# Performance work log

Measured on AMD Instinct MI355X. Metric: run time of the kernel, lower is better.

## Reference

```python
import jax, jax.numpy as jnp
import numpy as np

LN_EPS = 1e-6  # flax nn.LayerNorm default epsilon
NEG_SLOPE = 0.01  # jax.nn.leaky_relu default


def _layer_norm(x, scale, bias):
    m = jnp.mean(x, axis=-1, keepdims=True)
    v = jnp.mean(jnp.square(x - m), axis=-1, keepdims=True)
    return (x - m) * jax.lax.rsqrt(v + LN_EPS) * scale + bias


def setup_inputs() -> dict:
    key = jax.random.key(0)
    ks = jax.random.split(key, 10)
    B, D1, D2, OUT = 32768, 1024, 512, 1024
    inp = {
        "x1": jax.random.normal(ks[0], (B, D1), dtype=jnp.float32),
        "x2": jax.random.normal(ks[1], (B, D2), dtype=jnp.float32),
        # LayerNorm params (one per stream)
        "ln_scale1": jnp.ones((D1,), jnp.float32),
        "ln_bias1": jnp.zeros((D1,), jnp.float32),
        "ln_scale2": jnp.ones((D2,), jnp.float32),
        "ln_bias2": jnp.zeros((D2,), jnp.float32),
        # output Dense per stream: Dense(output_size)
        "W_out1": jax.random.normal(ks[2], (D1, OUT), jnp.float32) / np.sqrt(D1),
        "b_out1": jnp.zeros((OUT,), jnp.float32),
        "W_out2": jax.random.normal(ks[3], (D2, OUT), jnp.float32) / np.sqrt(D2),
        "b_out2": jnp.zeros((OUT,), jnp.float32),
        # gate Dense per stream: Dense(gate_size=output_size) for POINTWISE
        "W_g1": jax.random.normal(ks[4], (D1, OUT), jnp.float32) / np.sqrt(D1),
        "b_g1": jnp.zeros((OUT,), jnp.float32),
        "W_g2": jax.random.normal(ks[5], (D2, OUT), jnp.float32) / np.sqrt(D2),
        "b_g2": jnp.zeros((OUT,), jnp.float32),
    }
    return inp


def reference(x1, x2, ln_scale1, ln_bias1, ln_scale2, ln_bias2,
              W_out1, b_out1, W_out2, b_out2,
              W_g1, b_g1, W_g2, b_g2):
    # per-stream: LayerNorm -> leaky_relu -> Dense(output_size); pre-Dense
    # activation is also fed to the gate Dense.
    f1 = jax.nn.leaky_relu(_layer_norm(x1, ln_scale1, ln_bias1), NEG_SLOPE)
    f2 = jax.nn.leaky_relu(_layer_norm(x2, ln_scale2, ln_bias2), NEG_SLOPE)
    out1 = f1 @ W_out1 + b_out1  # [B, OUT]
    out2 = f2 @ W_out2 + b_out2  # [B, OUT]
    # two-stream POINTWISE gate: sum of gate Denses, sigmoid; the original
    # broadcasts gate [B,OUT] over stack([out1,out2]) and sums axis 0,
    # i.e. output = gate * (out1 + out2).
    gate = jax.nn.sigmoid((f1 @ W_g1 + b_g1) + (f2 @ W_g2 + b_g2))
    return gate * (out1 + out2)
```

## Files before the change

### kernel.cpp

```cpp
#include <hip/hip_runtime.h>
#include <hip/hip_bf16.h>
#include <stdint.h>

typedef __bf16 bf16x8 __attribute__((ext_vector_type(8)));
typedef float floatx4 __attribute__((ext_vector_type(4)));

__device__ __forceinline__ ushort f2bf(float f) {
  union { float f; uint32_t u; } v; v.f = f;
  uint32_t r = (v.u + 0x7fffu + ((v.u >> 16) & 1u)) >> 16;
  return (ushort)r;
}

__device__ __forceinline__ void load_lds16(const ushort* g, ushort* l) {
  __builtin_amdgcn_global_load_lds(
      (__attribute__((address_space(1))) void*)g,
      (__attribute__((address_space(3))) void*)l, 16, 0, 0);
}

__device__ __forceinline__ float leaky(float x) { return x >= 0.f ? x : 0.01f * x; }

__global__ __launch_bounds__(256) void ln2_kernel(
    const float* __restrict__ x1, const float* __restrict__ x2,
    const float* __restrict__ sc1p, const float* __restrict__ bi1p,
    const float* __restrict__ sc2p, const float* __restrict__ bi2p,
    ushort* __restrict__ f) {
  const int wid = (blockIdx.x << 2) + (threadIdx.x >> 6);
  const int lane = threadIdx.x & 63;

  float4 sc1[4], bi1[4], sc2[2], bi2[2];
#pragma unroll
  for (int j = 0; j < 4; j++) {
    sc1[j] = ((const float4*)sc1p)[j * 64 + lane];
    bi1[j] = ((const float4*)bi1p)[j * 64 + lane];
  }
#pragma unroll
  for (int j = 0; j < 2; j++) {
    sc2[j] = ((const float4*)sc2p)[j * 64 + lane];
    bi2[j] = ((const float4*)bi2p)[j * 64 + lane];
  }

#pragma unroll
  for (int it = 0; it < 2; ++it) {
    const int rA = wid + it * 16384;
    const int rB = rA + 8192;
    const float4* XA1 = (const float4*)(x1 + (size_t)rA * 1024);
    const float4* XA2 = (const float4*)(x2 + (size_t)rA * 512);
    const float4* XB1 = (const float4*)(x1 + (size_t)rB * 1024);
    const float4* XB2 = (const float4*)(x2 + (size_t)rB * 512);
    float4 a1[4], a2[2], b1[4], b2[2];
#pragma unroll
    for (int j = 0; j < 4; j++) a1[j] = XA1[j * 64 + lane];
#pragma unroll
    for (int j = 0; j < 2; j++) a2[j] = XA2[j * 64 + lane];
#pragma unroll
    for (int j = 0; j < 4; j++) b1[j] = XB1[j * 64 + lane];
#pragma unroll
    for (int j = 0; j < 2; j++) b2[j] = XB2[j * 64 + lane];

    float sA1 = 0.f, qA1 = 0.f, sA2 = 0.f, qA2 = 0.f;
    float sB1 = 0.f, qB1 = 0.f, sB2 = 0.f, qB2 = 0.f;
#pragma unroll
    for (int j = 0; j < 4; j++) {
      sA1 += a1[j].x + a1[j].y + a1[j].z + a1[j].w;
      qA1 += a1[j].x * a1[j].x + a1[j].y * a1[j].y + a1[j].z * a1[j].z + a1[j].w * a1[j].w;
      sB1 += b1[j].x + b1[j].y + b1[j].z + b1[j].w;
      qB1 += b1[j].x * b1[j].x + b1[j].y * b1[j].y + b1[j].z * b1[j].z + b1[j].w * b1[j].w;
    }
#pragma unroll
    for (int j = 0; j < 2; j++) {
      sA2 += a2[j].x + a2[j].y + a2[j].z + a2[j].w;
      qA2 += a2[j].x * a2[j].x + a2[j].y * a2[j].y + a2[j].z * a2[j].z + a2[j].w * a2[j].w;
      sB2 += b2[j].x + b2[j].y + b2[j].z + b2[j].w;
      qB2 += b2[j].x * b2[j].x + b2[j].y * b2[j].y + b2[j].z * b2[j].z + b2[j].w * b2[j].w;
    }
#pragma unroll
    for (int o = 1; o < 64; o <<= 1) {
      sA1 += __shfl_xor(sA1, o); qA1 += __shfl_xor(qA1, o);
      sA2 += __shfl_xor(sA2, o); qA2 += __shfl_xor(qA2, o);
      sB1 += __shfl_xor(sB1, o); qB1 += __shfl_xor(qB1, o);
      sB2 += __shfl_xor(sB2, o); qB2 += __shfl_xor(qB2, o);
    }
    const float mA1 = sA1 * (1.0f / 1024.0f);
    const float rA1 = rsqrtf(qA1 * (1.0f / 1024.0f) - mA1 * mA1 + 1e-6f);
    const float mA2 = sA2 * (1.0f / 512.0f);
    const float rA2v = rsqrtf(qA2 * (1.0f / 512.0f) - mA2 * mA2 + 1e-6f);
    const float mB1 = sB1 * (1.0f / 1024.0f);
    const float rB1 = rsqrtf(qB1 * (1.0f / 1024.0f) - mB1 * mB1 + 1e-6f);
    const float mB2 = sB2 * (1.0f / 512.0f);
    const float rB2v = rsqrtf(qB2 * (1.0f / 512.0f) - mB2 * mB2 + 1e-6f);

    ushort* fA = f + (size_t)rA * 1536;
    ushort* fB = f + (size_t)rB * 1536;
#pragma unroll
    for (int j = 0; j < 4; j++) {
      ushort4 oA, oB;
      oA.x = f2bf(leaky((a1[j].x - mA1) * rA1 * sc1[j].x + bi1[j].x));
      oA.y = f2bf(leaky((a1[j].y - mA1) * rA1 * sc1[j].y + bi1[j].y));
      oA.z = f2bf(leaky((a1[j].z - mA1) * rA1 * sc1[j].z + bi1[j].z));
      oA.w = f2bf(leaky((a1[j].w - mA1) * rA1 * sc1[j].w + bi1[j].w));
      oB.x = f2bf(leaky((b1[j].x - mB1) * rB1 * sc1[j].x + bi1[j].x));
      oB.y = f2bf(leaky((b1[j].y - mB1) * rB1 * sc1[j].y + bi1[j].y));
      oB.z = f2bf(leaky((b1[j].z - mB1) * rB1 * sc1[j].z + bi1[j].z));
      oB.w = f2bf(leaky((b1[j].w - mB1) * rB1 * sc1[j].w + bi1[j].w));
      ((ushort4*)fA)[j * 64 + lane] = oA;
      ((ushort4*)fB)[j * 64 + lane] = oB;
    }
#pragma unroll
    for (int j = 0; j < 2; j++) {
      ushort4 oA, oB;
      oA.x = f2bf(leaky((a2[j].x - mA2) * rA2v * sc2[j].x + bi2[j].x));
      oA.y = f2bf(leaky((a2[j].y - mA2) * rA2v * sc2[j].y + bi2[j].y));
      oA.z = f2bf(leaky((a2[j].z - mA2) * rA2v * sc2[j].z + bi2[j].z));
      oA.w = f2bf(leaky((a2[j].w - mA2) * rA2v * sc2[j].w + bi2[j].w));
      oB.x = f2bf(leaky((b2[j].x - mB2) * rB2v * sc2[j].x + bi2[j].x));
      oB.y = f2bf(leaky((b2[j].y - mB2) * rB2v * sc2[j].y + bi2[j].y));
      oB.z = f2bf(leaky((b2[j].z - mB2) * rB2v * sc2[j].z + bi2[j].z));
      oB.w = f2bf(leaky((b2[j].w - mB2) * rB2v * sc2[j].w + bi2[j].w));
      ((ushort4*)(fA + 1024))[j * 64 + lane] = oA;
      ((ushort4*)(fB + 1024))[j * 64 + lane] = oB;
    }
  }
}

__global__ __launch_bounds__(256) void wprep_kernel(
    const float* __restrict__ Wo1, const float* __restrict__ Wo2,
    const float* __restrict__ Wg1, const float* __restrict__ Wg2,
    ushort* __restrict__ WT) {
  __shared__ float tile[32][33];
  const int k0 = blockIdx.x * 32;
  const int j0 = blockIdx.y * 32;
  const int s = blockIdx.z;
  const float* Wa = s ? Wg1 : Wo1;
  const float* Wb = s ? Wg2 : Wo2;
  const int tx = threadIdx.x;
  const int ty = threadIdx.y;
#pragma unroll
  for (int r = 0; r < 4; r++) {
    const int k = k0 + ty + 8 * r;
    const float val = (k < 1024) ? Wa[(size_t)k * 1024 + j0 + tx]
                                 : Wb[(size_t)(k - 1024) * 1024 + j0 + tx];
    tile[ty + 8 * r][tx] = val;
  }
  __syncthreads();
#pragma unroll
  for (int r = 0; r < 4; r++) {
    const int j = j0 + ty + 8 * r;
    const int c = j & 63;
    const int n = (j >> 6) * 128 + (c >> 5) * 64 + s * 32 + ((c >> 4) & 1) * 16 + (c & 15);
    WT[(size_t)n * 1536 + k0 + tx] = f2bf(tile[tx][ty + 8 * r]);
  }
}

__global__ __launch_bounds__(512, 2) void gemm_fused(
    const ushort* __restrict__ A,
    const ushort* __restrict__ Bt,
    const float* __restrict__ bo1, const float* __restrict__ bo2,
    const float* __restrict__ bg1, const float* __restrict__ bg2,
    float* __restrict__ out) {
  __shared__ __align__(16) ushort As[2][16384];
  __shared__ __align__(16) ushort Bs[2][16384];
  const int orig = blockIdx.x;
  const int swz = (orig & 7) * 128 + (orig >> 3);
  const int mt = swz >> 3;
  const int nt = swz & 7;
  const int tid = threadIdx.x;
  const int wave = tid >> 6, lane = tid & 63;
  const int wr = wave >> 2, wcol = wave & 3;
  const int low = lane & 15, quad = lane >> 4;

  const int srow = wave * 8 + (lane >> 3);
  const int schunk = (lane & 7) ^ (lane >> 3);
  const ushort* gA0 = A + ((size_t)mt * 256 + srow) * 1536 + schunk * 8;
  const ushort* gB0 = Bt + ((size_t)nt * 256 + srow) * 1536 + schunk * 8;

  const int q2 = quad ^ (low & 3);
  const int kx = (low >> 2) & 1;
  const int offA_k0 = (wr * 128 + low) * 64 + (q2 + 4 * kx) * 8;
  const int offA_k1 = (wr * 128 + low) * 64 + (q2 + 4 * (1 - kx)) * 8;
  const int offB_k0 = (wcol * 64 + low) * 64 + (q2 + 4 * kx) * 8;
  const int offB_k1 = (wcol * 64 + low) * 64 + (q2 + 4 * (1 - kx)) * 8;

  floatx4 acc[8][4];
#pragma unroll
  for (int m = 0; m < 8; m++)
#pragma unroll
    for (int n = 0; n < 4; n++) acc[m][n] = (floatx4)0.0f;

#define STAGE_A(BUF, KT) do { \
    const ushort* s_ = gA0 + (KT) * 64; \
    ushort* d_ = &As[BUF][wave * 512]; \
    load_lds16(s_, d_); \
    load_lds16(s_ + 64 * 1536, d_ + 4096); \
    load_lds16(s_ + 128 * 1536, d_ + 8192); \
    load_lds16(s_ + 192 * 1536, d_ + 12288); \
  } while (0)
#define STAGE_B(BUF, KT) do { \
    const ushort* s_ = gB0 + (KT) * 64; \
    ushort* d_ = &Bs[BUF][wave * 512]; \
    load_lds16(s_, d_); \
    load_lds16(s_ + 64 * 1536, d_ + 4096); \
    load_lds16(s_ + 128 * 1536, d_ + 8192); \
    load_lds16(s_ + 192 * 1536, d_ + 12288); \
  } while (0)

  STAGE_A(0, 0);
  STAGE_B(0, 0);
  asm volatile("s_waitcnt vmcnt(0)" ::: "memory");
  __builtin_amdgcn_s_barrier();
  asm volatile("" ::: "memory");

#define TILE_STEP(CUR, T) do { \
    const ushort* Ac = &As[CUR][0]; \
    const ushort* Bc = &Bs[CUR][0]; \
    const bool pf = (T) < 23; \
    bf16x8 a[4], b[4]; \
     \
    _Pragma("unroll") for (int m = 0; m < 4; m++) a[m] = *(const bf16x8*)(Ac + offA_k0 + m * 1024); \
    _Pragma("unroll") for (int n = 0; n < 4; n++) b[n] = *(const bf16x8*)(Bc + offB_k0 + n * 1024); \
    if (pf) STAGE_A((CUR) ^ 1, (T) + 1); \
    asm volatile("" ::: "memory"); \
    __builtin_amdgcn_s_barrier(); \
    __builtin_amdgcn_s_setprio(1); \
    _Pragma("unroll") for (int m = 0; m < 4; m++) \
      _Pragma("unroll") for (int n = 0; n < 4; n++) \
        acc[m][n] = __builtin_amdgcn_mfma_f32_16x16x32_bf16(a[m], b[n], acc[m][n], 0, 0, 0); \
    __builtin_amdgcn_s_setprio(0); \
    asm volatile("" ::: "memory"); \
    __builtin_amdgcn_s_barrier(); \
     \
    _Pragma("unroll") for (int m = 0; m < 4; m++) a[m] = *(const bf16x8*)(Ac + offA_k0 + (m + 4) * 1024); \
    if (pf) STAGE_B((CUR) ^ 1, (T) + 1); \
    asm volatile("" ::: "memory"); \
    __builtin_amdgcn_s_barrier(); \
    __builtin_amdgcn_s_setprio(1); \
    _Pragma("unroll") for (int m = 0; m < 4; m++) \
      _Pragma("unroll") for (int n = 0; n < 4; n++) \
        acc[m + 4][n] = __builtin_amdgcn_mfma_f32_16x16x32_bf16(a[m], b[n], acc[m + 4][n], 0, 0, 0); \
    __builtin_amdgcn_s_setprio(0); \
    asm volatile("" ::: "memory"); \
    __builtin_amdgcn_s_barrier(); \
     \
    _Pragma("unroll") for (int m = 0; m < 4; m++) a[m] = *(const bf16x8*)(Ac + offA_k1 + m * 1024); \
    _Pragma("unroll") for (int n = 0; n < 4; n++) b[n] = *(const bf16x8*)(Bc + offB_k1 + n * 1024); \
    asm volatile("" ::: "memory"); \
    __builtin_amdgcn_s_barrier(); \
    __builtin_amdgcn_s_setprio(1); \
    _Pragma("unroll") for (int m = 0; m < 4; m++) \
      _Pragma("unroll") for (int n = 0; n < 4; n++) \
        acc[m][n] = __builtin_amdgcn_mfma_f32_16x16x32_bf16(a[m], b[n], acc[m][n], 0, 0, 0); \
    __builtin_amdgcn_s_setprio(0); \
    asm volatile("" ::: "memory"); \
    __builtin_amdgcn_s_barrier(); \
     \
    _Pragma("unroll") for (int m = 0; m < 4; m++) a[m] = *(const bf16x8*)(Ac + offA_k1 + (m + 4) * 1024); \
    asm volatile("" ::: "memory"); \
    __builtin_amdgcn_s_barrier(); \
    __builtin_amdgcn_s_setprio(1); \
    _Pragma("unroll") for (int m = 0; m < 4; m++) \
      _Pragma("unroll") for (int n = 0; n < 4; n++) \
        acc[m + 4][n] = __builtin_amdgcn_mfma_f32_16x16x32_bf16(a[m], b[n], acc[m + 4][n], 0, 0, 0); \
    __builtin_amdgcn_s_setprio(0); \
    asm volatile("s_waitcnt vmcnt(0)" ::: "memory"); \
    __builtin_amdgcn_s_barrier(); \
    asm volatile("" ::: "memory"); \
  } while (0)

  for (int tt = 0; tt < 12; tt++) {
    TILE_STEP(0, 2 * tt);
    TILE_STEP(1, 2 * tt + 1);
  }
#undef TILE_STEP
#undef STAGE_A
#undef STAGE_B

  const int colbase = (nt * 4 + wcol) << 5;
#pragma unroll
  for (int n = 0; n < 2; n++) {
    const int col = colbase + n * 16 + low;
    const float bs = bo1[col] + bo2[col];
    const float bg = bg1[col] + bg2[col];
#pragma unroll
    for (int m = 0; m < 8; m++) {
      const floatx4 S = acc[m][n];
      const floatx4 G = acc[m][n + 2];
      const size_t rb = (size_t)mt * 256 + wr * 128 + m * 16 + quad * 4;
#pragma unroll
      for (int r = 0; r < 4; r++) {
        const float sv = S[r] + bs;
        const float gv = G[r] + bg;
        const float gate = 1.0f / (1.0f + __expf(-gv));
        out[(rb + r) * 1024 + col] = gate * sv;
      }
    }
  }
}

extern "C" void kernel_launch(void* const* d_in, const int* in_sizes, int n_in,
                              void* d_out, int out_size, void* d_ws, size_t ws_size,
                              hipStream_t stream) {
  const float* x1 = (const float*)d_in[0];
  const float* x2 = (const float*)d_in[1];
  const float* ln_s1 = (const float*)d_in[2];
  const float* ln_b1 = (const float*)d_in[3];
  const float* ln_s2 = (const float*)d_in[4];
  const float* ln_b2 = (const float*)d_in[5];
  const float* W_out1 = (const float*)d_in[6];
  const float* b_out1 = (const float*)d_in[7];
  const float* W_out2 = (const float*)d_in[8];
  const float* b_out2 = (const float*)d_in[9];
  const float* W_g1 = (const float*)d_in[10];
  const float* b_g1 = (const float*)d_in[11];
  const float* W_g2 = (const float*)d_in[12];
  const float* b_g2 = (const float*)d_in[13];
  float* out = (float*)d_out;

  ushort* f = (ushort*)d_ws;
  ushort* WT = f + (size_t)32768 * 1536;

  ln2_kernel<<<2048, 256, 0, stream>>>(x1, x2, ln_s1, ln_b1, ln_s2, ln_b2, f);
  wprep_kernel<<<dim3(48, 32, 2), dim3(32, 8), 0, stream>>>(W_out1, W_out2, W_g1, W_g2, WT);
  gemm_fused<<<dim3(1024), dim3(512), 0, stream>>>(f, WT, b_out1, b_out2, b_g1, b_g2, out);
}
```

Baseline: 518.4 us.

## Fuse LayerNorm apply into GEMM A-staging, keep only per-row stats pass

Replaces the LayerNorm kernel that wrote a bf16 activation matrix with a stats-only kernel that stores per-row mean and rstd. The GEMM now loads raw fp32 x1/x2 rows, applies normalization, leaky ReLU and bf16 packing in registers, and writes the result into LDS instead of using async global-to-LDS loads. This removes the write and re-read of the bf16 intermediate. In exchange, the GEMM reads fp32 A once per N tile (8 times, twice the bytes of bf16) and adds VALU work and register pressure to the main loop.

```diff
diff --git a/kernel.cpp b/kernel.cpp
--- a/kernel.cpp
+++ b/kernel.cpp
@@ -4,6 +4,7 @@
 
 typedef __bf16 bf16x8 __attribute__((ext_vector_type(8)));
 typedef float floatx4 __attribute__((ext_vector_type(4)));
+typedef unsigned short u16x8v __attribute__((ext_vector_type(8)));
 
 __device__ __forceinline__ ushort f2bf(float f) {
   union { float f; uint32_t u; } v; v.f = f;
@@ -19,26 +20,25 @@
 
 __device__ __forceinline__ float leaky(float x) { return x >= 0.f ? x : 0.01f * x; }
 
-__global__ __launch_bounds__(256) void ln2_kernel(
+__device__ __forceinline__ u16x8v lnpack(float4 xa, float4 xb, float4 sa, float4 sb,
+                                         float4 ba, float4 bb, float m, float rv) {
+  u16x8v o;
+  o[0] = f2bf(leaky((xa.x - m) * rv * sa.x + ba.x));
+  o[1] = f2bf(leaky((xa.y - m) * rv * sa.y + ba.y));
+  o[2] = f2bf(leaky((xa.z - m) * rv * sa.z + ba.z));
+  o[3] = f2bf(leaky((xa.w - m) * rv * sa.w + ba.w));
+  o[4] = f2bf(leaky((xb.x - m) * rv * sb.x + bb.x));
+  o[5] = f2bf(leaky((xb.y - m) * rv * sb.y + bb.y));
+  o[6] = f2bf(leaky((xb.z - m) * rv * sb.z + bb.z));
+  o[7] = f2bf(leaky((xb.w - m) * rv * sb.w + bb.w));
+  return o;
+}
+
+__global__ __launch_bounds__(256) void stats_kernel(
     const float* __restrict__ x1, const float* __restrict__ x2,
-    const float* __restrict__ sc1p, const float* __restrict__ bi1p,
-    const float* __restrict__ sc2p, const float* __restrict__ bi2p,
-    ushort* __restrict__ f) {
+    float* __restrict__ stats) {
   const int wid = (blockIdx.x << 2) + (threadIdx.x >> 6);
   const int lane = threadIdx.x & 63;
-
-  float4 sc1[4], bi1[4], sc2[2], bi2[2];
-#pragma unroll
-  for (int j = 0; j < 4; j++) {
-    sc1[j] = ((const float4*)sc1p)[j * 64 + lane];
-    bi1[j] = ((const float4*)bi1p)[j * 64 + lane];
-  }
-#pragma unroll
-  for (int j = 0; j < 2; j++) {
-    sc2[j] = ((const float4*)sc2p)[j * 64 + lane];
-    bi2[j] = ((const float4*)bi2p)[j * 64 + lane];
-  }
-
 #pragma unroll
   for (int it = 0; it < 2; ++it) {
     const int rA = wid + it * 16384;
@@ -47,31 +47,25 @@
     const float4* XA2 = (const float4*)(x2 + (size_t)rA * 512);
     const float4* XB1 = (const float4*)(x1 + (size_t)rB * 1024);
     const float4* XB2 = (const float4*)(x2 + (size_t)rB * 512);
-    float4 a1[4], a2[2], b1[4], b2[2];
-#pragma unroll
-    for (int j = 0; j < 4; j++) a1[j] = XA1[j * 64 + lane];
-#pragma unroll
-    for (int j = 0; j < 2; j++) a2[j] = XA2[j * 64 + lane];
-#pragma unroll
-    for (int j = 0; j < 4; j++) b1[j] = XB1[j * 64 + lane];
-#pragma unroll
-    for (int j = 0; j < 2; j++) b2[j] = XB2[j * 64 + lane];
-
     float sA1 = 0.f, qA1 = 0.f, sA2 = 0.f, qA2 = 0.f;
     float sB1 = 0.f, qB1 = 0.f, sB2 = 0.f, qB2 = 0.f;
 #pragma unroll
     for (int j = 0; j < 4; j++) {
-      sA1 += a1[j].x + a1[j].y + a1[j].z + a1[j].w;
-      qA1 += a1[j].x * a1[j].x + a1[j].y * a1[j].y + a1[j].z * a1[j].z + a1[j].w * a1[j].w;
-      sB1 += b1[j].x + b1[j].y + b1[j].z + b1[j].w;
-      qB1 += b1[j].x * b1[j].x + b1[j].y * b1[j].y + b1[j].z * b1[j].z + b1[j].w * b1[j].w;
+      const float4 a = XA1[j * 64 + lane];
+      const float4 b = XB1[j * 64 + lane];
+      sA1 += a.x + a.y + a.z + a.w;
+      qA1 += a.x * a.x + a.y * a.y + a.z * a.z + a.w * a.w;
+      sB1 += b.x + b.y + b.z + b.w;
+      qB1 += b.x * b.x + b.y * b.y + b.z * b.z + b.w * b.w;
     }
 #pragma unroll
     for (int j = 0; j < 2; j++) {
-      sA2 += a2[j].x + a2[j].y + a2[j].z + a2[j].w;
-      qA2 += a2[j].x * a2[j].x + a2[j].y * a2[j].y + a2[j].z * a2[j].z + a2[j].w * a2[j].w;
-      sB2 += b2[j].x + b2[j].y + b2[j].z + b2[j].w;
-      qB2 += b2[j].x * b2[j].x + b2[j].y * b2[j].y + b2[j].z * b2[j].z + b2[j].w * b2[j].w;
+      const float4 a = XA2[j * 64 + lane];
+      const float4 b = XB2[j * 64 + lane];
+      sA2 += a.x + a.y + a.z + a.w;
+      qA2 += a.x * a.x + a.y * a.y + a.z * a.z + a.w * a.w;
+      sB2 += b.x + b.y + b.z + b.w;
+      qB2 += b.x * b.x + b.y * b.y + b.z * b.z + b.w * b.w;
     }
 #pragma unroll
     for (int o = 1; o < 64; o <<= 1) {
@@ -80,44 +74,17 @@
       sB1 += __shfl_xor(sB1, o); qB1 += __shfl_xor(qB1, o);
       sB2 += __shfl_xor(sB2, o); qB2 += __shfl_xor(qB2, o);
     }
-    const float mA1 = sA1 * (1.0f / 1024.0f);
-    const float rA1 = rsqrtf(qA1 * (1.0f / 1024.0f) - mA1 * mA1 + 1e-6f);
-    const float mA2 = sA2 * (1.0f / 512.0f);
-    const float rA2v = rsqrtf(qA2 * (1.0f / 512.0f) - mA2 * mA2 + 1e-6f);
-    const float mB1 = sB1 * (1.0f / 1024.0f);
-    const float rB1 = rsqrtf(qB1 * (1.0f / 1024.0f) - mB1 * mB1 + 1e-6f);
-    const float mB2 = sB2 * (1.0f / 512.0f);
-    const float rB2v = rsqrtf(qB2 * (1.0f / 512.0f) - mB2 * mB2 + 1e-6f);
-
-    ushort* fA = f + (size_t)rA * 1536;
-    ushort* fB = f + (size_t)rB * 1536;
-#pragma unroll
-    for (int j = 0; j < 4; j++) {
-      ushort4 oA, oB;
-      oA.x = f2bf(leaky((a1[j].x - mA1) * rA1 * sc1[j].x + bi1[j].x));
-      oA.y = f2bf(leaky((a1[j].y - mA1) * rA1 * sc1[j].y + bi1[j].y));
-      oA.z = f2bf(leaky((a1[j].z - mA1) * rA1 * sc1[j].z + bi1[j].z));
-      oA.w = f2bf(leaky((a1[j].w - mA1) * rA1 * sc1[j].w + bi1[j].w));
-      oB.x = f2bf(leaky((b1[j].x - mB1) * rB1 * sc1[j].x + bi1[j].x));
-      oB.y = f2bf(leaky((b1[j].y - mB1) * rB1 * sc1[j].y + bi1[j].y));
-      oB.z = f2bf(leaky((b1[j].z - mB1) * rB1 * sc1[j].z + bi1[j].z));
-      oB.w = f2bf(leaky((b1[j].w - mB1) * rB1 * sc1[j].w + bi1[j].w));
-      ((ushort4*)fA)[j * 64 + lane] = oA;
-      ((ushort4*)fB)[j * 64 + lane] = oB;
-    }
-#pragma unroll
-    for (int j = 0; j < 2; j++) {
-      ushort4 oA, oB;
-      oA.x = f2bf(leaky((a2[j].x - mA2) * rA2v * sc2[j].x + bi2[j].x));
-      oA.y = f2bf(leaky((a2[j].y - mA2) * rA2v * sc2[j].y + bi2[j].y));
-      oA.z = f2bf(leaky((a2[j].z - mA2) * rA2v * sc2[j].z + bi2[j].z));
-      oA.w = f2bf(leaky((a2[j].w - mA2) * rA2v * sc2[j].w + bi2[j].w));
-      oB.x = f2bf(leaky((b2[j].x - mB2) * rB2v * sc2[j].x + bi2[j].x));
-      oB.y = f2bf(leaky((b2[j].y - mB2) * rB2v * sc2[j].y + bi2[j].y));
-      oB.z = f2bf(leaky((b2[j].z - mB2) * rB2v * sc2[j].z + bi2[j].z));
-      oB.w = f2bf(leaky((b2[j].w - mB2) * rB2v * sc2[j].w + bi2[j].w));
-      ((ushort4*)(fA + 1024))[j * 64 + lane] = oA;
-      ((ushort4*)(fB + 1024))[j * 64 + lane] = oB;
+    if (lane == 0) {
+      const float mA1 = sA1 * (1.0f / 1024.0f);
+      const float vA1 = rsqrtf(qA1 * (1.0f / 1024.0f) - mA1 * mA1 + 1e-6f);
+      const float mA2 = sA2 * (1.0f / 512.0f);
+      const float vA2 = rsqrtf(qA2 * (1.0f / 512.0f) - mA2 * mA2 + 1e-6f);
+      const float mB1 = sB1 * (1.0f / 1024.0f);
+      const float vB1 = rsqrtf(qB1 * (1.0f / 1024.0f) - mB1 * mB1 + 1e-6f);
+      const float mB2 = sB2 * (1.0f / 512.0f);
+      const float vB2 = rsqrtf(qB2 * (1.0f / 512.0f) - mB2 * mB2 + 1e-6f);
+      ((float4*)stats)[rA] = make_float4(mA1, vA1, mA2, vA2);
+      ((float4*)stats)[rB] = make_float4(mB1, vB1, mB2, vB2);
     }
   }
 }
@@ -152,13 +119,17 @@
 }
 
 __global__ __launch_bounds__(512, 2) void gemm_fused(
-    const ushort* __restrict__ A,
+    const float* __restrict__ x1, const float* __restrict__ x2,
+    const float* __restrict__ sc1p, const float* __restrict__ bi1p,
+    const float* __restrict__ sc2p, const float* __restrict__ bi2p,
+    const float* __restrict__ stats,
     const ushort* __restrict__ Bt,
     const float* __restrict__ bo1, const float* __restrict__ bo2,
     const float* __restrict__ bg1, const float* __restrict__ bg2,
     float* __restrict__ out) {
   __shared__ __align__(16) ushort As[2][16384];
   __shared__ __align__(16) ushort Bs[2][16384];
+  __shared__ __align__(16) float statsL[256][4];
   const int orig = blockIdx.x;
   const int swz = (orig & 7) * 128 + (orig >> 3);
   const int mt = swz >> 3;
@@ -168,10 +139,18 @@
   const int wr = wave >> 2, wcol = wave & 3;
   const int low = lane & 15, quad = lane >> 4;
 
+  const size_t arow0 = (size_t)mt * 256;
   const int srow = wave * 8 + (lane >> 3);
   const int schunk = (lane & 7) ^ (lane >> 3);
-  const ushort* gA0 = A + ((size_t)mt * 256 + srow) * 1536 + schunk * 8;
   const ushort* gB0 = Bt + ((size_t)nt * 256 + srow) * 1536 + schunk * 8;
+
+  const float* xr1[4];
+  const float* xr2[4];
+#pragma unroll
+  for (int s = 0; s < 4; s++) {
+    xr1[s] = x1 + (arow0 + srow + 64 * s) * 1024 + schunk * 8;
+    xr2[s] = x2 + (arow0 + srow + 64 * s) * 512 + schunk * 8;
+  }
 
   const int q2 = quad ^ (low & 3);
   const int kx = (low >> 2) & 1;
@@ -186,14 +165,19 @@
 #pragma unroll
     for (int n = 0; n < 4; n++) acc[m][n] = (floatx4)0.0f;
 
-#define STAGE_A(BUF, KT) do { \
-    const ushort* s_ = gA0 + (KT) * 64; \
-    ushort* d_ = &As[BUF][wave * 512]; \
-    load_lds16(s_, d_); \
-    load_lds16(s_ + 64 * 1536, d_ + 4096); \
-    load_lds16(s_ + 128 * 1536, d_ + 8192); \
-    load_lds16(s_ + 192 * 1536, d_ + 12288); \
+#define STAGE_A2(NB, S0, ST1_, KO_, SA, SB, BA, BB) do { \
+    const float* ps0_ = ((ST1_) ? xr1[S0] : xr2[S0]) + (KO_); \
+    const float* ps1_ = ((ST1_) ? xr1[(S0) + 1] : xr2[(S0) + 1]) + (KO_); \
+    const float4 x0a_ = ((const float4*)ps0_)[0], x0b_ = ((const float4*)ps0_)[1]; \
+    const float4 x1a_ = ((const float4*)ps1_)[0], x1b_ = ((const float4*)ps1_)[1]; \
+    const float2 mr0_ = *(const float2*)&statsL[srow + 64 * (S0)][(ST1_) ? 0 : 2]; \
+    const float2 mr1_ = *(const float2*)&statsL[srow + 64 * ((S0) + 1)][(ST1_) ? 0 : 2]; \
+    const u16x8v o0_ = lnpack(x0a_, x0b_, SA, SB, BA, BB, mr0_.x, mr0_.y); \
+    const u16x8v o1_ = lnpack(x1a_, x1b_, SA, SB, BA, BB, mr1_.x, mr1_.y); \
+    *(u16x8v*)(&As[NB][wave * 512 + (S0) * 4096 + lane * 8]) = o0_; \
+    *(u16x8v*)(&As[NB][wave * 512 + ((S0) + 1) * 4096 + lane * 8]) = o1_; \
   } while (0)
+
 #define STAGE_B(BUF, KT) do { \
     const ushort* s_ = gB0 + (KT) * 64; \
     ushort* d_ = &Bs[BUF][wave * 512]; \
@@ -203,40 +187,61 @@
     load_lds16(s_ + 192 * 1536, d_ + 12288); \
   } while (0)
 
-  STAGE_A(0, 0);
-  STAGE_B(0, 0);
-  asm volatile("s_waitcnt vmcnt(0)" ::: "memory");
+  if (tid < 256) *(float4*)&statsL[tid][0] = ((const float4*)stats)[arow0 + tid];
+  {
+    const float* scp = sc1p + schunk * 8;
+    const float* bip = bi1p + schunk * 8;
+    const float4 sa = ((const float4*)scp)[0], sb = ((const float4*)scp)[1];
+    const float4 ba = ((const float4*)bip)[0], bb = ((const float4*)bip)[1];
+    STAGE_B(0, 0);
+    asm volatile("s_waitcnt lgkmcnt(0)" ::: "memory");
+    __builtin_amdgcn_s_barrier();
+    STAGE_A2(0, 0, true, 0, sa, sb, ba, bb);
+    STAGE_A2(0, 2, true, 0, sa, sb, ba, bb);
+  }
+  asm volatile("s_waitcnt vmcnt(0) lgkmcnt(0)" ::: "memory");
   __builtin_amdgcn_s_barrier();
   asm volatile("" ::: "memory");
+
+#define MFMA16(MBASE) do { \
+    __builtin_amdgcn_s_setprio(1); \
+    _Pragma("unroll") for (int m = 0; m < 4; m++) \
+      _Pragma("unroll") for (int n = 0; n < 4; n++) \
+        acc[m + (MBASE)][n] = __builtin_amdgcn_mfma_f32_16x16x32_bf16(a[m], b[n], acc[m + (MBASE)][n], 0, 0, 0); \
+    __builtin_amdgcn_s_setprio(0); \
+  } while (0)
 
 #define TILE_STEP(CUR, T) do { \
     const ushort* Ac = &As[CUR][0]; \
     const ushort* Bc = &Bs[CUR][0]; \
     const bool pf = (T) < 23; \
+    const int ktn = (T) + 1; \
+    const bool st1 = ktn < 16; \
+    const int ko = (st1 ? ktn : ktn - 16) * 64; \
+    float4 sa, sb, ba, bb; \
+    if (pf) { \
+      const float* scp = (st1 ? sc1p : sc2p) + ko + schunk * 8; \
+      const float* bip = (st1 ? bi1p : bi2p) + ko + schunk * 8; \
+      sa = ((const float4*)scp)[0]; sb = ((const float4*)scp)[1]; \
+      ba = ((const float4*)bip)[0]; bb = ((const float4*)bip)[1]; \
+    } \
     bf16x8 a[4], b[4]; \
      \
+    if (pf) STAGE_A2((CUR) ^ 1, 0, st1, ko, sa, sb, ba, bb); \
     _Pragma("unroll") for (int m = 0; m < 4; m++) a[m] = *(const bf16x8*)(Ac + offA_k0 + m * 1024); \
     _Pragma("unroll") for (int n = 0; n < 4; n++) b[n] = *(const bf16x8*)(Bc + offB_k0 + n * 1024); \
-    if (pf) STAGE_A((CUR) ^ 1, (T) + 1); \
-    asm volatile("" ::: "memory"); \
-    __builtin_amdgcn_s_barrier(); \
-    __builtin_amdgcn_s_setprio(1); \
-    _Pragma("unroll") for (int m = 0; m < 4; m++) \
-      _Pragma("unroll") for (int n = 0; n < 4; n++) \
-        acc[m][n] = __builtin_amdgcn_mfma_f32_16x16x32_bf16(a[m], b[n], acc[m][n], 0, 0, 0); \
-    __builtin_amdgcn_s_setprio(0); \
+    asm volatile("" ::: "memory"); \
+    __builtin_amdgcn_s_barrier(); \
+    MFMA16(0); \
     asm volatile("" ::: "memory"); \
     __builtin_amdgcn_s_barrier(); \
      \
+    if (pf) STAGE_A2((CUR) ^ 1, 2, st1, ko, sa, sb, ba, bb); \
+    if (pf) STAGE_B((CUR) ^ 1, ktn); \
     _Pragma("unroll") for (int m = 0; m < 4; m++) a[m] = *(const bf16x8*)(Ac + offA_k0 + (m + 4) * 1024); \
-    if (pf) STAGE_B((CUR) ^ 1, (T) + 1); \
-    asm volatile("" ::: "memory"); \
-    __builtin_amdgcn_s_barrier(); \
-    __builtin_amdgcn_s_setprio(1); \
-    _Pragma("unroll") for (int m = 0; m < 4; m++) \
-      _Pragma("unroll") for (int n = 0; n < 4; n++) \
-        acc[m + 4][n] = __builtin_amdgcn_mfma_f32_16x16x32_bf16(a[m], b[n], acc[m + 4][n], 0, 0, 0); \
-    __builtin_amdgcn_s_setprio(0); \
+    asm volatile("" ::: "memory"); \
+    __builtin_amdgcn_s_barrier(); \
+    MFMA16(4); \
     asm volatile("" ::: "memory"); \
     __builtin_amdgcn_s_barrier(); \
      \
@@ -244,23 +249,15 @@
     _Pragma("unroll") for (int n = 0; n < 4; n++) b[n] = *(const bf16x8*)(Bc + offB_k1 + n * 1024); \
     asm volatile("" ::: "memory"); \
     __builtin_amdgcn_s_barrier(); \
-    __builtin_amdgcn_s_setprio(1); \
-    _Pragma("unroll") for (int m = 0; m < 4; m++) \
-      _Pragma("unroll") for (int n = 0; n < 4; n++) \
-        acc[m][n] = __builtin_amdgcn_mfma_f32_16x16x32_bf16(a[m], b[n], acc[m][n], 0, 0, 0); \
-    __builtin_amdgcn_s_setprio(0); \
+    MFMA16(0); \
     asm volatile("" ::: "memory"); \
     __builtin_amdgcn_s_barrier(); \
      \
     _Pragma("unroll") for (int m = 0; m < 4; m++) a[m] = *(const bf16x8*)(Ac + offA_k1 + (m + 4) * 1024); \
     asm volatile("" ::: "memory"); \
     __builtin_amdgcn_s_barrier(); \
-    __builtin_amdgcn_s_setprio(1); \
-    _Pragma("unroll") for (int m = 0; m < 4; m++) \
-      _Pragma("unroll") for (int n = 0; n < 4; n++) \
-        acc[m + 4][n] = __builtin_amdgcn_mfma_f32_16x16x32_bf16(a[m], b[n], acc[m + 4][n], 0, 0, 0); \
-    __builtin_amdgcn_s_setprio(0); \
-    asm volatile("s_waitcnt vmcnt(0)" ::: "memory"); \
+    MFMA16(4); \
+    asm volatile("s_waitcnt vmcnt(0) lgkmcnt(0)" ::: "memory"); \
     __builtin_amdgcn_s_barrier(); \
     asm volatile("" ::: "memory"); \
   } while (0)
@@ -270,7 +267,8 @@
     TILE_STEP(1, 2 * tt + 1);
   }
 #undef TILE_STEP
-#undef STAGE_A
+#undef MFMA16
+#undef STAGE_A2
 #undef STAGE_B
 
   const int colbase = (nt * 4 + wcol) << 5;
@@ -314,10 +312,12 @@
   const float* b_g2 = (const float*)d_in[13];
   float* out = (float*)d_out;
 
-  ushort* f = (ushort*)d_ws;
-  ushort* WT = f + (size_t)32768 * 1536;
-
-  ln2_kernel<<<2048, 256, 0, stream>>>(x1, x2, ln_s1, ln_b1, ln_s2, ln_b2, f);
+  ushort* WT = (ushort*)d_ws;
+  float* stats = (float*)((char*)d_ws + 6291456);
+
+  stats_kernel<<<2048, 256, 0, stream>>>(x1, x2, stats);
   wprep_kernel<<<dim3(48, 32, 2), dim3(32, 8), 0, stream>>>(W_out1, W_out2, W_g1, W_g2, WT);
-  gemm_fused<<<dim3(1024), dim3(512), 0, stream>>>(f, WT, b_out1, b_out2, b_g1, b_g2, out);
-}
+  gemm_fused<<<dim3(1024), dim3(512), 0, stream>>>(
+      x1, x2, ln_s1, ln_b1, ln_s2, ln_b2, stats, WT,
+      b_out1, b_out2, b_g1, b_g2, out);
+}
```

Result: slower. 677.9 us (+30.8%).

## Triple-buffer B tiles and prefetch two K-steps ahead with partial vmcnt waits

Applied to the files above, without the earlier changes.

Adds a third LDS buffer for the B operand so B tiles are staged two K-iterations ahead while A stays double-buffered. The end-of-step wait changes from a full vmcnt(0) drain to vmcnt(4), so the next B tile's global-to-LDS loads stay in flight across the barrier. This is meant to hide more global load latency behind MFMA work. In exchange it raises LDS use to 160KB per block and fully unrolls the 24-step K loop, which grows code size.

```diff
diff --git a/kernel.cpp b/kernel.cpp
--- a/kernel.cpp
+++ b/kernel.cpp
@@ -158,7 +158,7 @@
     const float* __restrict__ bg1, const float* __restrict__ bg2,
     float* __restrict__ out) {
   __shared__ __align__(16) ushort As[2][16384];
-  __shared__ __align__(16) ushort Bs[2][16384];
+  __shared__ __align__(16) ushort Bs[3][16384];
   const int orig = blockIdx.x;
   const int swz = (orig & 7) * 128 + (orig >> 3);
   const int mt = swz >> 3;
@@ -186,90 +186,86 @@
 #pragma unroll
     for (int n = 0; n < 4; n++) acc[m][n] = (floatx4)0.0f;
 
-#define STAGE_A(BUF, KT) do { \
+#define STAGE_A(NB, KT) do { \
     const ushort* s_ = gA0 + (KT) * 64; \
-    ushort* d_ = &As[BUF][wave * 512]; \
+    ushort* d_ = &As[NB][wave * 512]; \
     load_lds16(s_, d_); \
     load_lds16(s_ + 64 * 1536, d_ + 4096); \
     load_lds16(s_ + 128 * 1536, d_ + 8192); \
     load_lds16(s_ + 192 * 1536, d_ + 12288); \
   } while (0)
-#define STAGE_B(BUF, KT) do { \
+#define STAGE_B(NB, KT) do { \
     const ushort* s_ = gB0 + (KT) * 64; \
-    ushort* d_ = &Bs[BUF][wave * 512]; \
+    ushort* d_ = &Bs[NB][wave * 512]; \
     load_lds16(s_, d_); \
     load_lds16(s_ + 64 * 1536, d_ + 4096); \
     load_lds16(s_ + 128 * 1536, d_ + 8192); \
     load_lds16(s_ + 192 * 1536, d_ + 12288); \
   } while (0)
 
+#define MFMA16(MBASE) do { \
+    __builtin_amdgcn_s_setprio(1); \
+    _Pragma("unroll") for (int m_ = 0; m_ < 4; m_++) \
+      _Pragma("unroll") for (int n_ = 0; n_ < 4; n_++) \
+        acc[m_ + (MBASE)][n_] = __builtin_amdgcn_mfma_f32_16x16x32_bf16(a[m_], b[n_], acc[m_ + (MBASE)][n_], 0, 0, 0); \
+    __builtin_amdgcn_s_setprio(0); \
+  } while (0)
+
   STAGE_A(0, 0);
   STAGE_B(0, 0);
-  asm volatile("s_waitcnt vmcnt(0)" ::: "memory");
+  STAGE_B(1, 1);
+  asm volatile("s_waitcnt vmcnt(4)" ::: "memory");
   __builtin_amdgcn_s_barrier();
   asm volatile("" ::: "memory");
 
-#define TILE_STEP(CUR, T) do { \
-    const ushort* Ac = &As[CUR][0]; \
-    const ushort* Bc = &Bs[CUR][0]; \
-    const bool pf = (T) < 23; \
-    bf16x8 a[4], b[4]; \
-     \
-    _Pragma("unroll") for (int m = 0; m < 4; m++) a[m] = *(const bf16x8*)(Ac + offA_k0 + m * 1024); \
-    _Pragma("unroll") for (int n = 0; n < 4; n++) b[n] = *(const bf16x8*)(Bc + offB_k0 + n * 1024); \
-    if (pf) STAGE_A((CUR) ^ 1, (T) + 1); \
-    asm volatile("" ::: "memory"); \
-    __builtin_amdgcn_s_barrier(); \
-    __builtin_amdgcn_s_setprio(1); \
-    _Pragma("unroll") for (int m = 0; m < 4; m++) \
-      _Pragma("unroll") for (int n = 0; n < 4; n++) \
-        acc[m][n] = __builtin_amdgcn_mfma_f32_16x16x32_bf16(a[m], b[n], acc[m][n], 0, 0, 0); \
-    __builtin_amdgcn_s_setprio(0); \
-    asm volatile("" ::: "memory"); \
-    __builtin_amdgcn_s_barrier(); \
-     \
-    _Pragma("unroll") for (int m = 0; m < 4; m++) a[m] = *(const bf16x8*)(Ac + offA_k0 + (m + 4) * 1024); \
-    if (pf) STAGE_B((CUR) ^ 1, (T) + 1); \
-    asm volatile("" ::: "memory"); \
-    __builtin_amdgcn_s_barrier(); \
-    __builtin_amdgcn_s_setprio(1); \
-    _Pragma("unroll") for (int m = 0; m < 4; m++) \
-      _Pragma("unroll") for (int n = 0; n < 4; n++) \
-        acc[m + 4][n] = __builtin_amdgcn_mfma_f32_16x16x32_bf16(a[m], b[n], acc[m + 4][n], 0, 0, 0); \
-    __builtin_amdgcn_s_setprio(0); \
-    asm volatile("" ::: "memory"); \
-    __builtin_amdgcn_s_barrier(); \
-     \
-    _Pragma("unroll") for (int m = 0; m < 4; m++) a[m] = *(const bf16x8*)(Ac + offA_k1 + m * 1024); \
-    _Pragma("unroll") for (int n = 0; n < 4; n++) b[n] = *(const bf16x8*)(Bc + offB_k1 + n * 1024); \
-    asm volatile("" ::: "memory"); \
-    __builtin_amdgcn_s_barrier(); \
-    __builtin_amdgcn_s_setprio(1); \
-    _Pragma("unroll") for (int m = 0; m < 4; m++) \
-      _Pragma("unroll") for (int n = 0; n < 4; n++) \
-        acc[m][n] = __builtin_amdgcn_mfma_f32_16x16x32_bf16(a[m], b[n], acc[m][n], 0, 0, 0); \
-    __builtin_amdgcn_s_setprio(0); \
-    asm volatile("" ::: "memory"); \
-    __builtin_amdgcn_s_barrier(); \
-     \
-    _Pragma("unroll") for (int m = 0; m < 4; m++) a[m] = *(const bf16x8*)(Ac + offA_k1 + (m + 4) * 1024); \
-    asm volatile("" ::: "memory"); \
-    __builtin_amdgcn_s_barrier(); \
-    __builtin_amdgcn_s_setprio(1); \
-    _Pragma("unroll") for (int m = 0; m < 4; m++) \
-      _Pragma("unroll") for (int n = 0; n < 4; n++) \
-        acc[m + 4][n] = __builtin_amdgcn_mfma_f32_16x16x32_bf16(a[m], b[n], acc[m + 4][n], 0, 0, 0); \
-    __builtin_amdgcn_s_setprio(0); \
-    asm volatile("s_waitcnt vmcnt(0)" ::: "memory"); \
-    __builtin_amdgcn_s_barrier(); \
-    asm volatile("" ::: "memory"); \
-  } while (0)
-
-  for (int tt = 0; tt < 12; tt++) {
-    TILE_STEP(0, 2 * tt);
-    TILE_STEP(1, 2 * tt + 1);
-  }
-#undef TILE_STEP
+#pragma unroll
+  for (int t = 0; t < 24; ++t) {
+    const ushort* Ac = &As[t & 1][0];
+    const ushort* Bc = &Bs[t % 3][0];
+    bf16x8 a[4], b[4];
+#pragma unroll
+    for (int m = 0; m < 4; m++) a[m] = *(const bf16x8*)(Ac + offA_k0 + m * 1024);
+#pragma unroll
+    for (int n = 0; n < 4; n++) b[n] = *(const bf16x8*)(Bc + offB_k0 + n * 1024);
+    if (t < 23) STAGE_A((t + 1) & 1, t + 1);
+    asm volatile("" ::: "memory");
+    __builtin_amdgcn_s_barrier();
+    MFMA16(0);
+    asm volatile("" ::: "memory");
+    __builtin_amdgcn_s_barrier();
+#pragma unroll
+    for (int m = 0; m < 4; m++) a[m] = *(const bf16x8*)(Ac + offA_k0 + (m + 4) * 1024);
+    if (t < 22) STAGE_B((t + 2) % 3, t + 2);
+    asm volatile("" ::: "memory");
+    __builtin_amdgcn_s_barrier();
+    MFMA16(4);
+    asm volatile("" ::: "memory");
+    __builtin_amdgcn_s_barrier();
+#pragma unroll
+    for (int m = 0; m < 4; m++) a[m] = *(const bf16x8*)(Ac + offA_k1 + m * 1024);
+#pragma unroll
+    for (int n = 0; n < 4; n++) b[n] = *(const bf16x8*)(Bc + offB_k1 + n * 1024);
+    asm volatile("" ::: "memory");
+    __builtin_amdgcn_s_barrier();
+    MFMA16(0);
+    asm volatile("" ::: "memory");
+    __builtin_amdgcn_s_barrier();
+#pragma unroll
+    for (int m = 0; m < 4; m++) a[m] = *(const bf16x8*)(Ac + offA_k1 + (m + 4) * 1024);
+    asm volatile("" ::: "memory");
+    __builtin_amdgcn_s_barrier();
+    MFMA16(4);
+    if (t < 22) {
+      asm volatile("s_waitcnt vmcnt(4)" ::: "memory");
+      __builtin_amdgcn_s_barrier();
+      asm volatile("" ::: "memory");
+    } else if (t == 22) {
+      asm volatile("s_waitcnt vmcnt(0)" ::: "memory");
+      __builtin_amdgcn_s_barrier();
+      asm volatile("" ::: "memory");
+    }
+  }
+#undef MFMA16
 #undef STAGE_A
 #undef STAGE_B
 
```

Measured after the change: 519.1 us. Within noise of the previous version (+0.1%).
